# Optimization experiments

Hardware: AMD Instinct MI355X
Metric: run time of the kernel (lower is better)

## Reference

```python
import jax, jax.numpy as jnp
import numpy as np

D_MODEL = 256
N_HEAD = 4
HEAD_DIM = D_MODEL // N_HEAD  # 64


def setup_inputs() -> dict:
    key = jax.random.key(0)
    kx, kw, kb = jax.random.split(key, 3)
    x = jax.random.normal(kx, (4, 2048, D_MODEL), dtype=jnp.float32)
    # nn.Linear(256, 768): weight [768, 256], bias [768]
    bound = 1.0 / np.sqrt(D_MODEL)
    W_qkv = jax.random.uniform(kw, (3 * D_MODEL, D_MODEL), dtype=jnp.float32, minval=-bound, maxval=bound)
    b_qkv = jax.random.uniform(kb, (3 * D_MODEL,), dtype=jnp.float32, minval=-bound, maxval=bound)
    return {"x": x, "W_qkv": W_qkv, "b_qkv": b_qkv}


def reference(x, W_qkv, b_qkv):
    B, S, _ = x.shape
    # fused QKV projection: [B, S, 3*D]
    qkv = jnp.einsum("bsd,ed->bse", x, W_qkv) + b_qkv
    q, k, v = jnp.split(qkv, 3, axis=-1)
    # [B, S, D] -> [B, H, S, Dh]
    def to_heads(t):
        return t.reshape(B, S, N_HEAD, HEAD_DIM).transpose(0, 2, 1, 3)
    q, k, v = to_heads(q), to_heads(k), to_heads(v)
    scale = 1.0 / np.sqrt(HEAD_DIM)
    # scores [B, H, S, S]
    scores = jnp.einsum("bhqd,bhkd->bhqk", q, k) * scale
    attn = jax.nn.softmax(scores, axis=-1)
    out = jnp.einsum("bhqk,bhkd->bhqd", attn, v)  # [B, H, S, Dh]
    return out
```

## Files before the change

### kernel.cpp

```cpp
#include <hip/hip_runtime.h>

#define BB 4
#define SS 2048
#define DM 256
#define NH 4
#define DH 64
#define NROW (BB*SS)
#define NE   (3*DM)
#define BH   (BB*NH)
#define HEAD_ELEMS (BH*SS*DH)
#define NQROWS (BH*SS)
#define NKZ 4

typedef _Float16 half_t;
typedef __attribute__((ext_vector_type(8))) _Float16 half8;
typedef __attribute__((ext_vector_type(4))) _Float16 half4;
typedef __attribute__((ext_vector_type(4))) float floatx4;

#define KPAD 72

#define QK_SCALE 0.18033688011112042f
#define EXP2(x) __builtin_amdgcn_exp2f(x)
#define DEFER_THR 8.0f

__global__ __launch_bounds__(256) void prep(const float* __restrict__ x,
                                            const float* __restrict__ W,
                                            half_t* __restrict__ xh,
                                            half_t* __restrict__ xl,
                                            half_t* __restrict__ wh) {
    int gtid = blockIdx.x * 256 + threadIdx.x;
    {
        int i = gtid * 4;
        float4 v = *(const float4*)&x[i];
        half4 h, l;
        h.x = (half_t)v.x; l.x = (half_t)(v.x - (float)h.x);
        h.y = (half_t)v.y; l.y = (half_t)(v.y - (float)h.y);
        h.z = (half_t)v.z; l.z = (half_t)(v.z - (float)h.z);
        h.w = (half_t)v.w; l.w = (half_t)(v.w - (float)h.w);
        *(half4*)&xh[i] = h;
        *(half4*)&xl[i] = l;
    }
    if (gtid < NE * DM / 4) {
        int i = gtid * 4;
        float4 v = *(const float4*)&W[i];
        half4 h;
        h.x = (half_t)v.x; h.y = (half_t)v.y;
        h.z = (half_t)v.z; h.w = (half_t)v.w;
        *(half4*)&wh[i] = h;
    }
}

__global__ __launch_bounds__(256) void qkv_proj(const half_t* __restrict__ xh,
                                                const half_t* __restrict__ xl,
                                                const half_t* __restrict__ whg,
                                                const float* __restrict__ bias,
                                                half_t* __restrict__ qh,
                                                half_t* __restrict__ kh,
                                                half_t* __restrict__ vt) {
    __shared__ __align__(16) half_t Xh[64 * KPAD];
    __shared__ __align__(16) half_t Xl[64 * KPAD];
    __shared__ __align__(16) half_t Wh[64 * KPAD];

    const int rb   = blockIdx.x * 64;
    const int nb   = blockIdx.y * 64;
    const int tid  = threadIdx.x;
    const int wid  = tid >> 6;
    const int lane = tid & 63;
    const int quad = lane >> 4;
    const int col  = lane & 15;

    floatx4 acc[4];
    #pragma unroll
    for (int t = 0; t < 4; ++t) acc[t] = (floatx4){0.f, 0.f, 0.f, 0.f};

    for (int k0 = 0; k0 < DM; k0 += 64) {
        __syncthreads();
        #pragma unroll
        for (int i = 0; i < 2; ++i) {
            int gi = tid + 256 * i;
            int r  = gi >> 3;
            int c8 = (gi & 7) * 8;
            *(half8*)&Xh[r * KPAD + c8] = *(const half8*)&xh[(size_t)(rb + r) * DM + k0 + c8];
            *(half8*)&Xl[r * KPAD + c8] = *(const half8*)&xl[(size_t)(rb + r) * DM + k0 + c8];
            *(half8*)&Wh[r * KPAD + c8] = *(const half8*)&whg[(size_t)(nb + r) * DM + k0 + c8];
        }
        __syncthreads();

        half8 ah0 = *(const half8*)&Xh[(wid * 16 + col) * KPAD + quad * 8];
        half8 ah1 = *(const half8*)&Xh[(wid * 16 + col) * KPAD + 32 + quad * 8];
        half8 al0 = *(const half8*)&Xl[(wid * 16 + col) * KPAD + quad * 8];
        half8 al1 = *(const half8*)&Xl[(wid * 16 + col) * KPAD + 32 + quad * 8];

        #pragma unroll
        for (int t = 0; t < 4; ++t) {
            half8 bh0 = *(const half8*)&Wh[(t * 16 + col) * KPAD + quad * 8];
            half8 bh1 = *(const half8*)&Wh[(t * 16 + col) * KPAD + 32 + quad * 8];
            acc[t] = __builtin_amdgcn_mfma_f32_16x16x32_f16(ah0, bh0, acc[t], 0, 0, 0);
            acc[t] = __builtin_amdgcn_mfma_f32_16x16x32_f16(ah1, bh1, acc[t], 0, 0, 0);
            acc[t] = __builtin_amdgcn_mfma_f32_16x16x32_f16(al0, bh0, acc[t], 0, 0, 0);
            acc[t] = __builtin_amdgcn_mfma_f32_16x16x32_f16(al1, bh1, acc[t], 0, 0, 0);
        }
    }

    const int part = nb >> 8;
    const int mloc = wid * 16 + quad * 4;
    if (part != 2) {
        #pragma unroll
        for (int t = 0; t < 4; ++t) {
            int e    = nb + t * 16 + col;
            float be = bias[e];
            int dm   = e & 255;
            int h    = dm >> 6;
            int dh   = dm & 63;
            #pragma unroll
            for (int r = 0; r < 4; ++r) {
                int row = rb + mloc + r;
                int b   = row >> 11;
                int s   = row & 2047;
                int bh_ = b * NH + h;
                float val = acc[t][r] + be;
                if (part == 0) {
                    qh[((size_t)bh_ * SS + s) * DH + dh] = (half_t)(val * QK_SCALE);
                } else {
                    kh[((size_t)bh_ * SS + s) * DH + dh] = (half_t)val;
                }
            }
        }
    } else {
        __syncthreads();
        #pragma unroll
        for (int t = 0; t < 4; ++t) {
            int e    = nb + t * 16 + col;
            float be = bias[e];
            #pragma unroll
            for (int r = 0; r < 4; ++r)
                Xh[(t * 16 + col) * KPAD + mloc + r] = (half_t)(acc[t][r] + be);
        }
        __syncthreads();
        const int b   = rb >> 11;
        const int s0  = rb & 2047;
        const int h   = (nb >> 6) & 3;
        const int bh_ = b * NH + h;
        #pragma unroll
        for (int i = 0; i < 2; ++i) {
            int idx = tid + 256 * i;
            int rr  = idx >> 3;
            int cc8 = (idx & 7) * 8;
            *(half8*)&vt[((size_t)bh_ * DH + rr) * SS + s0 + cc8] =
                *(const half8*)&Xh[rr * KPAD + cc8];
        }
    }
}

__global__ __launch_bounds__(256, 4) void attn(const half_t* __restrict__ qh,
                                               const half_t* __restrict__ kh,
                                               const half_t* __restrict__ vt,
                                               half_t* __restrict__ pO,
                                               float* __restrict__ mst,
                                               float* __restrict__ lst) {
    __shared__ __align__(16) half_t Ks[64 * KPAD];
    __shared__ __align__(16) half_t Vts[64 * KPAD];

    const int lin  = blockIdx.x + 32 * (blockIdx.y + 16 * blockIdx.z);
    const int xcd  = lin & 7;
    const int j    = lin >> 3;
    const int strm = xcd + 8 * (j >> 5);
    const int q0   = (j & 31) * 64;
    const int bh   = strm & 15;
    const int kz   = strm >> 4;

    const size_t base = (size_t)bh * SS * DH;
    const int tid  = threadIdx.x;
    const int wid  = tid >> 6;
    const int lane = tid & 63;
    const int quad = lane >> 4;
    const int col  = lane & 15;
    const int ktBeg = kz * (SS / NKZ);
    const int ktEnd = ktBeg + (SS / NKZ);

    int srr[2], scc[2];
    #pragma unroll
    for (int i = 0; i < 2; ++i) {
        int gi = tid + 256 * i;
        srr[i] = gi >> 3;
        scc[i] = (gi & 7) * 8;
    }

    half8 bq0, bq1;
    {
        int s = q0 + wid * 16 + col;
        bq0 = *(const half8*)&qh[base + (size_t)s * DH + quad * 8];
        bq1 = *(const half8*)&qh[base + (size_t)s * DH + 32 + quad * 8];
    }

    half8 nk[2], nv[2];
    #pragma unroll
    for (int i = 0; i < 2; ++i) {
        nk[i] = *(const half8*)&kh[base + (size_t)(ktBeg + srr[i]) * DH + scc[i]];
        nv[i] = *(const half8*)&vt[base + (size_t)srr[i] * SS + ktBeg + scc[i]];
    }

    float m_i = -3.0e38f;
    float l_part = 0.f;
    floatx4 o[4];
    #pragma unroll
    for (int dt = 0; dt < 4; ++dt) o[dt] = (floatx4){0.f, 0.f, 0.f, 0.f};

    for (int kt = ktBeg; kt < ktEnd; kt += 64) {
        __syncthreads();
        #pragma unroll
        for (int i = 0; i < 2; ++i) {
            *(half8*)&Ks[srr[i] * KPAD + scc[i]]  = nk[i];
            *(half8*)&Vts[srr[i] * KPAD + scc[i]] = nv[i];
        }
        __syncthreads();

        const int ktn = kt + 64;
        if (ktn < ktEnd) {
            #pragma unroll
            for (int i = 0; i < 2; ++i) {
                nk[i] = *(const half8*)&kh[base + (size_t)(ktn + srr[i]) * DH + scc[i]];
                nv[i] = *(const half8*)&vt[base + (size_t)srr[i] * SS + ktn + scc[i]];
            }
        }

        floatx4 sc[4];
        #pragma unroll
        for (int t = 0; t < 4; ++t) {
            half8 ak0 = *(const half8*)&Ks[(t * 16 + col) * KPAD + quad * 8];
            half8 ak1 = *(const half8*)&Ks[(t * 16 + col) * KPAD + 32 + quad * 8];
            floatx4 c = (floatx4){0.f, 0.f, 0.f, 0.f};
            c = __builtin_amdgcn_mfma_f32_16x16x32_f16(ak0, bq0, c, 0, 0, 0);
            c = __builtin_amdgcn_mfma_f32_16x16x32_f16(ak1, bq1, c, 0, 0, 0);
            sc[t] = c;
        }

        float mloc = -3.0e38f;
        #pragma unroll
        for (int t = 0; t < 4; ++t) {
            float a = fmaxf(fmaxf(sc[t][0], sc[t][1]), fmaxf(sc[t][2], sc[t][3]));
            mloc = fmaxf(mloc, a);
        }
        mloc = fmaxf(mloc, __shfl_xor(mloc, 16));
        mloc = fmaxf(mloc, __shfl_xor(mloc, 32));

        bool skip = __all(mloc <= m_i + DEFER_THR);
        float m_new = skip ? m_i : fmaxf(m_i, mloc);

        half4 pa[4];
        float rsumL = 0.f;
        #pragma unroll
        for (int t = 0; t < 4; ++t) {
            float p0 = EXP2(sc[t][0] - m_new);
            float p1 = EXP2(sc[t][1] - m_new);
            float p2 = EXP2(sc[t][2] - m_new);
            float p3 = EXP2(sc[t][3] - m_new);
            rsumL += p0 + p1 + p2 + p3;
            pa[t] = (half4){(half_t)p0, (half_t)p1, (half_t)p2, (half_t)p3};
        }

        if (skip) {
            l_part += rsumL;
        } else {
            float alpha = EXP2(m_i - m_new);
            m_i = m_new;
            l_part = l_part * alpha + rsumL;
            float ar[4];
            #pragma unroll
            for (int i = 0; i < 4; ++i) ar[i] = __shfl(alpha, quad * 4 + i);
            #pragma unroll
            for (int dt = 0; dt < 4; ++dt)
                #pragma unroll
                for (int i = 0; i < 4; ++i)
                    o[dt][i] *= ar[i];
        }

        #pragma unroll
        for (int t = 0; t < 4; ++t) {
            #pragma unroll
            for (int dt = 0; dt < 4; ++dt) {
                half4 bv = *(const half4*)&Vts[(dt * 16 + col) * KPAD + t * 16 + quad * 4];
                o[dt] = __builtin_amdgcn_mfma_f32_16x16x16f16(pa[t], bv, o[dt], 0, 0, 0);
            }
        }
    }

    float l_i = l_part + __shfl_xor(l_part, 16);
    l_i += __shfl_xor(l_i, 32);

    const size_t pbase = (size_t)kz * HEAD_ELEMS + base;
    {
        float inv = 1.0f / l_i;
        float ir[4];
        #pragma unroll
        for (int i = 0; i < 4; ++i) ir[i] = __shfl(inv, quad * 4 + i);
        #pragma unroll
        for (int dt = 0; dt < 4; ++dt)
            #pragma unroll
            for (int i = 0; i < 4; ++i) {
                int row = q0 + wid * 16 + quad * 4 + i;
                pO[pbase + (size_t)row * DH + dt * 16 + col] = (half_t)(o[dt][i] * ir[i]);
            }
        if (quad == 0) {
            int row = q0 + wid * 16 + col;
            int idx = kz * NQROWS + bh * SS + row;
            mst[idx] = m_i;
            lst[idx] = l_i;
        }
    }
}

__global__ __launch_bounds__(256) void merge(const half_t* __restrict__ pO,
                                             const float* __restrict__ mst,
                                             const float* __restrict__ lst,
                                             float* __restrict__ out) {
    int gid = blockIdx.x * 256 + threadIdx.x;
    int row = gid >> 3;
    int dc  = (gid & 7) * 8;
    float m[NKZ], l[NKZ];
    #pragma unroll
    for (int p = 0; p < NKZ; ++p) {
        m[p] = mst[p * NQROWS + row];
        l[p] = lst[p * NQROWS + row];
    }
    float M = fmaxf(fmaxf(m[0], m[1]), fmaxf(m[2], m[3]));
    float w[NKZ], wsum = 0.f;
    #pragma unroll
    for (int p = 0; p < NKZ; ++p) { w[p] = l[p] * EXP2(m[p] - M); wsum += w[p]; }
    float inv = 1.0f / wsum;

    float r[8] = {0.f,0.f,0.f,0.f,0.f,0.f,0.f,0.f};
    #pragma unroll
    for (int p = 0; p < NKZ; ++p) {
        float a = w[p] * inv;
        half8 ov = *(const half8*)&pO[(size_t)p * HEAD_ELEMS + (size_t)row * DH + dc];
        #pragma unroll
        for (int e = 0; e < 8; ++e) r[e] += a * (float)ov[e];
    }
    float4 r0 = {r[0], r[1], r[2], r[3]};
    float4 r1 = {r[4], r[5], r[6], r[7]};
    *(float4*)&out[(size_t)row * DH + dc]     = r0;
    *(float4*)&out[(size_t)row * DH + dc + 4] = r1;
}

extern "C" void kernel_launch(void* const* d_in, const int* in_sizes, int n_in,
                              void* d_out, int out_size, void* d_ws, size_t ws_size,
                              hipStream_t stream) {
    const float* x  = (const float*)d_in[0];
    const float* Wq = (const float*)d_in[1];
    const float* bq = (const float*)d_in[2];
    float* out = (float*)d_out;

    half_t* qh  = (half_t*)d_ws;
    half_t* kh  = qh + (size_t)HEAD_ELEMS;
    half_t* vt  = kh + (size_t)HEAD_ELEMS;
    half_t* xh  = vt + (size_t)HEAD_ELEMS;
    half_t* xl  = xh + (size_t)HEAD_ELEMS;
    half_t* whp = xl + (size_t)HEAD_ELEMS;
    half_t* pO  = (half_t*)d_ws + (size_t)6 * HEAD_ELEMS;
    float*  mst = (float*)((char*)d_ws + (size_t)10 * HEAD_ELEMS * 2);
    float*  lst = mst + (size_t)NKZ * NQROWS;

    prep<<<2048, 256, 0, stream>>>(x, Wq, xh, xl, whp);
    qkv_proj<<<dim3(NROW / 64, NE / 64), 256, 0, stream>>>(xh, xl, whp, bq, qh, kh, vt);
    attn<<<dim3(SS / 64, BH, NKZ), 256, 0, stream>>>(qh, kh, vt, pO, mst, lst);
    merge<<<1024, 256, 0, stream>>>(pO, mst, lst, out);
}
```

Before: 115.5 us.

## Process two 16-row query subtiles per wave to reuse K/V tiles

```diff
diff --git a/kernel.cpp b/kernel.cpp
--- a/kernel.cpp
+++ b/kernel.cpp
@@ -152,20 +152,20 @@
     }
 }
 
-__global__ __launch_bounds__(256, 4) void attn(const half_t* __restrict__ qh,
-                                               const half_t* __restrict__ kh,
-                                               const half_t* __restrict__ vt,
-                                               half_t* __restrict__ pO,
-                                               float* __restrict__ mst,
-                                               float* __restrict__ lst) {
+__global__ __launch_bounds__(256) void attn(const half_t* __restrict__ qh,
+                                            const half_t* __restrict__ kh,
+                                            const half_t* __restrict__ vt,
+                                            half_t* __restrict__ pO,
+                                            float* __restrict__ mst,
+                                            float* __restrict__ lst) {
     __shared__ __align__(16) half_t Ks[64 * KPAD];
     __shared__ __align__(16) half_t Vts[64 * KPAD];
 
-    const int lin  = blockIdx.x + 32 * (blockIdx.y + 16 * blockIdx.z);
+    const int lin  = blockIdx.x + 16 * blockIdx.y + 256 * blockIdx.z;
     const int xcd  = lin & 7;
     const int j    = lin >> 3;
-    const int strm = xcd + 8 * (j >> 5);
-    const int q0   = (j & 31) * 64;
+    const int strm = xcd + 8 * (j >> 4);
+    const int q0   = (j & 15) * 128;
     const int bh   = strm & 15;
     const int kz   = strm >> 4;
 
@@ -186,11 +186,12 @@
         scc[i] = (gi & 7) * 8;
     }
 
-    half8 bq0, bq1;
-    {
-        int s = q0 + wid * 16 + col;
-        bq0 = *(const half8*)&qh[base + (size_t)s * DH + quad * 8];
-        bq1 = *(const half8*)&qh[base + (size_t)s * DH + 32 + quad * 8];
+    half8 bq[2][2];
+    #pragma unroll
+    for (int st = 0; st < 2; ++st) {
+        int s = q0 + wid * 32 + st * 16 + col;
+        bq[st][0] = *(const half8*)&qh[base + (size_t)s * DH + quad * 8];
+        bq[st][1] = *(const half8*)&qh[base + (size_t)s * DH + 32 + quad * 8];
     }
 
     half8 nk[2], nv[2];
@@ -200,11 +201,13 @@
         nv[i] = *(const half8*)&vt[base + (size_t)srr[i] * SS + ktBeg + scc[i]];
     }
 
-    float m_i = -3.0e38f;
-    float l_part = 0.f;
-    floatx4 o[4];
-    #pragma unroll
-    for (int dt = 0; dt < 4; ++dt) o[dt] = (floatx4){0.f, 0.f, 0.f, 0.f};
+    float m_i[2]    = {-3.0e38f, -3.0e38f};
+    float l_part[2] = {0.f, 0.f};
+    floatx4 o[2][4];
+    #pragma unroll
+    for (int st = 0; st < 2; ++st)
+        #pragma unroll
+        for (int dt = 0; dt < 4; ++dt) o[st][dt] = (floatx4){0.f, 0.f, 0.f, 0.f};
 
     for (int kt = ktBeg; kt < ktEnd; kt += 64) {
         __syncthreads();
@@ -224,55 +227,62 @@
             }
         }
 
-        floatx4 sc[4];
+        floatx4 sc[2][4];
         #pragma unroll
         for (int t = 0; t < 4; ++t) {
             half8 ak0 = *(const half8*)&Ks[(t * 16 + col) * KPAD + quad * 8];
             half8 ak1 = *(const half8*)&Ks[(t * 16 + col) * KPAD + 32 + quad * 8];
-            floatx4 c = (floatx4){0.f, 0.f, 0.f, 0.f};
-            c = __builtin_amdgcn_mfma_f32_16x16x32_f16(ak0, bq0, c, 0, 0, 0);
-            c = __builtin_amdgcn_mfma_f32_16x16x32_f16(ak1, bq1, c, 0, 0, 0);
-            sc[t] = c;
-        }
-
-        float mloc = -3.0e38f;
-        #pragma unroll
-        for (int t = 0; t < 4; ++t) {
-            float a = fmaxf(fmaxf(sc[t][0], sc[t][1]), fmaxf(sc[t][2], sc[t][3]));
-            mloc = fmaxf(mloc, a);
-        }
-        mloc = fmaxf(mloc, __shfl_xor(mloc, 16));
-        mloc = fmaxf(mloc, __shfl_xor(mloc, 32));
-
-        bool skip = __all(mloc <= m_i + DEFER_THR);
-        float m_new = skip ? m_i : fmaxf(m_i, mloc);
-
-        half4 pa[4];
-        float rsumL = 0.f;
-        #pragma unroll
-        for (int t = 0; t < 4; ++t) {
-            float p0 = EXP2(sc[t][0] - m_new);
-            float p1 = EXP2(sc[t][1] - m_new);
-            float p2 = EXP2(sc[t][2] - m_new);
-            float p3 = EXP2(sc[t][3] - m_new);
-            rsumL += p0 + p1 + p2 + p3;
-            pa[t] = (half4){(half_t)p0, (half_t)p1, (half_t)p2, (half_t)p3};
-        }
-
-        if (skip) {
-            l_part += rsumL;
-        } else {
-            float alpha = EXP2(m_i - m_new);
-            m_i = m_new;
-            l_part = l_part * alpha + rsumL;
-            float ar[4];
-            #pragma unroll
-            for (int i = 0; i < 4; ++i) ar[i] = __shfl(alpha, quad * 4 + i);
-            #pragma unroll
-            for (int dt = 0; dt < 4; ++dt)
+            #pragma unroll
+            for (int st = 0; st < 2; ++st) {
+                floatx4 c = (floatx4){0.f, 0.f, 0.f, 0.f};
+                c = __builtin_amdgcn_mfma_f32_16x16x32_f16(ak0, bq[st][0], c, 0, 0, 0);
+                c = __builtin_amdgcn_mfma_f32_16x16x32_f16(ak1, bq[st][1], c, 0, 0, 0);
+                sc[st][t] = c;
+            }
+        }
+
+        half4 pa[2][4];
+        #pragma unroll
+        for (int st = 0; st < 2; ++st) {
+            float mloc = -3.0e38f;
+            #pragma unroll
+            for (int t = 0; t < 4; ++t) {
+                float a = fmaxf(fmaxf(sc[st][t][0], sc[st][t][1]),
+                                fmaxf(sc[st][t][2], sc[st][t][3]));
+                mloc = fmaxf(mloc, a);
+            }
+            mloc = fmaxf(mloc, __shfl_xor(mloc, 16));
+            mloc = fmaxf(mloc, __shfl_xor(mloc, 32));
+
+            bool skip = __all(mloc <= m_i[st] + DEFER_THR);
+            float m_new = skip ? m_i[st] : fmaxf(m_i[st], mloc);
+
+            float rsumL = 0.f;
+            #pragma unroll
+            for (int t = 0; t < 4; ++t) {
+                float p0 = EXP2(sc[st][t][0] - m_new);
+                float p1 = EXP2(sc[st][t][1] - m_new);
+                float p2 = EXP2(sc[st][t][2] - m_new);
+                float p3 = EXP2(sc[st][t][3] - m_new);
+                rsumL += p0 + p1 + p2 + p3;
+                pa[st][t] = (half4){(half_t)p0, (half_t)p1, (half_t)p2, (half_t)p3};
+            }
+
+            if (skip) {
+                l_part[st] += rsumL;
+            } else {
+                float alpha = EXP2(m_i[st] - m_new);
+                m_i[st] = m_new;
+                l_part[st] = l_part[st] * alpha + rsumL;
+                float ar[4];
                 #pragma unroll
-                for (int i = 0; i < 4; ++i)
-                    o[dt][i] *= ar[i];
+                for (int i = 0; i < 4; ++i) ar[i] = __shfl(alpha, quad * 4 + i);
+                #pragma unroll
+                for (int dt = 0; dt < 4; ++dt)
+                    #pragma unroll
+                    for (int i = 0; i < 4; ++i)
+                        o[st][dt][i] *= ar[i];
+            }
         }
 
         #pragma unroll
@@ -280,16 +290,18 @@
             #pragma unroll
             for (int dt = 0; dt < 4; ++dt) {
                 half4 bv = *(const half4*)&Vts[(dt * 16 + col) * KPAD + t * 16 + quad * 4];
-                o[dt] = __builtin_amdgcn_mfma_f32_16x16x16f16(pa[t], bv, o[dt], 0, 0, 0);
-            }
-        }
-    }
-
-    float l_i = l_part + __shfl_xor(l_part, 16);
-    l_i += __shfl_xor(l_i, 32);
+                #pragma unroll
+                for (int st = 0; st < 2; ++st)
+                    o[st][dt] = __builtin_amdgcn_mfma_f32_16x16x16f16(pa[st][t], bv, o[st][dt], 0, 0, 0);
+            }
+        }
+    }
 
     const size_t pbase = (size_t)kz * HEAD_ELEMS + base;
-    {
+    #pragma unroll
+    for (int st = 0; st < 2; ++st) {
+        float l_i = l_part[st] + __shfl_xor(l_part[st], 16);
+        l_i += __shfl_xor(l_i, 32);
         float inv = 1.0f / l_i;
         float ir[4];
         #pragma unroll
@@ -298,13 +310,13 @@
         for (int dt = 0; dt < 4; ++dt)
             #pragma unroll
             for (int i = 0; i < 4; ++i) {
-                int row = q0 + wid * 16 + quad * 4 + i;
-                pO[pbase + (size_t)row * DH + dt * 16 + col] = (half_t)(o[dt][i] * ir[i]);
+                int row = q0 + wid * 32 + st * 16 + quad * 4 + i;
+                pO[pbase + (size_t)row * DH + dt * 16 + col] = (half_t)(o[st][dt][i] * ir[i]);
             }
         if (quad == 0) {
-            int row = q0 + wid * 16 + col;
+            int row = q0 + wid * 32 + st * 16 + col;
             int idx = kz * NQROWS + bh * SS + row;
-            mst[idx] = m_i;
+            mst[idx] = m_i[st];
             lst[idx] = l_i;
         }
     }
@@ -363,6 +375,6 @@
 
     prep<<<2048, 256, 0, stream>>>(x, Wq, xh, xl, whp);
     qkv_proj<<<dim3(NROW / 64, NE / 64), 256, 0, stream>>>(xh, xl, whp, bq, qh, kh, vt);
-    attn<<<dim3(SS / 64, BH, NKZ), 256, 0, stream>>>(qh, kh, vt, pO, mst, lst);
+    attn<<<dim3(SS / 128, BH, NKZ), 256, 0, stream>>>(qh, kh, vt, pO, mst, lst);
     merge<<<1024, 256, 0, stream>>>(pO, mst, lst, out);
 }
```

New measurement: 113.7 us. Within noise of the previous version (-1.6%).
